# Kernel tuning notes

Hardware: AMD Instinct MI355X
Metric: run time of the kernel (lower is better)

Reference implementation:

```python
import jax, jax.numpy as jnp
import numpy as np

VOL = 64          # self.vol_size
SPACE = 0.2       # space_size (cubic), space_center = 0
IMG = 255.0       # normalization constant in the source (2*u/255 - 1)


def setup_inputs() -> dict:
    key = jax.random.key(0)
    ks = jax.random.split(key, 5)
    B, V, C, Hf, Wf = 2, 4, 32, 64, 64
    features = jax.random.normal(ks[0], (B, V, C, Hf, Wf), jnp.float32)
    # near-identity rotations, cameras ~0.5m away, focal ~200, principal point 128
    camera_R = jnp.eye(3, dtype=jnp.float32)[None, None] + 0.01 * jax.random.normal(ks[1], (B, V, 3, 3), jnp.float32)
    camera_T = jnp.array([0.0, 0.0, 0.5], jnp.float32) + 0.01 * jax.random.normal(ks[2], (B, V, 3), jnp.float32)
    K0 = jnp.array([[200.0, 0.0, 128.0], [0.0, 200.0, 128.0], [0.0, 0.0, 1.0]], jnp.float32)
    Kmask = jnp.array([[1.0, 0.0, 1.0], [0.0, 1.0, 1.0], [0.0, 0.0, 0.0]], jnp.float32)
    camera_K = K0[None, None] + 0.5 * jax.random.normal(ks[3], (B, V, 3, 3), jnp.float32) * Kmask
    root_world = 0.01 * jax.random.normal(ks[4], (B, 3), jnp.float32)
    return dict(features=features, camera_R=camera_R, camera_T=camera_T,
                camera_K=camera_K, root_world=root_world)


def _bilinear_sample(feat, x, y):
    """PyTorch F.grid_sample, mode=bilinear, padding=zeros, align_corners=False.
    feat: [N,C,H,W]; x,y: [N,P] pixel-space coords (already unnormalized).
    Returns [N,C,P]."""
    N, C, H, W = feat.shape
    x0 = jnp.floor(x); y0 = jnp.floor(y)
    x1 = x0 + 1.0;     y1 = y0 + 1.0
    wx1 = x - x0; wx0 = 1.0 - wx1
    wy1 = y - y0; wy0 = 1.0 - wy1
    feat_flat = feat.reshape(N, C, H * W)

    def gather(xi, yi, w):
        valid = (xi >= 0) & (xi <= W - 1) & (yi >= 0) & (yi <= H - 1)
        xi_c = jnp.clip(xi, 0, W - 1).astype(jnp.int32)
        yi_c = jnp.clip(yi, 0, H - 1).astype(jnp.int32)
        idx = yi_c * W + xi_c                                   # [N,P]
        vals = jnp.take_along_axis(feat_flat, idx[:, None, :], axis=2)  # [N,C,P]
        return vals * (w * valid.astype(feat.dtype))[:, None, :]

    return (gather(x0, y0, wx0 * wy0) + gather(x1, y0, wx1 * wy0)
            + gather(x0, y1, wx0 * wy1) + gather(x1, y1, wx1 * wy1))


def reference(features, camera_R, camera_T, camera_K, root_world):
    B, V, C, Hf, Wf = features.shape
    D = VOL
    # _build_grid: 64^3 points, xyz order, spanning SPACE around center 0
    r = jnp.arange(D, dtype=jnp.float32)
    z, y, x = jnp.meshgrid(r, r, r, indexing='ij')
    grid = jnp.stack([x, y, z], axis=0) / (D - 1)               # [3,D,D,D]
    pts = ((grid - 0.5) * SPACE).reshape(3, -1).T               # [P,3], P = D^3
    # relative camera translation: new_T = R @ root + T
    new_T = jnp.einsum('bvij,bj->bvi', camera_R, root_world) + camera_T
    # project: pts_cam = pts @ R^T + T  -> [B,V,P,3]
    pts_cam = jnp.einsum('pj,bvij->bvpi', pts, camera_R) + new_T[:, :, None, :]
    zc = jnp.maximum(pts_cam[..., 2], 1e-5)
    fx = camera_K[:, :, 0, 0][..., None]; fy = camera_K[:, :, 1, 1][..., None]
    cx = camera_K[:, :, 0, 2][..., None]; cy = camera_K[:, :, 1, 2][..., None]
    u = pts_cam[..., 0] * fx / zc + cx
    v = pts_cam[..., 1] * fy / zc + cy
    u_n = 2.0 * u / IMG - 1.0
    v_n = 2.0 * v / IMG - 1.0
    # unnormalize (align_corners=False): ix = ((g+1)*W - 1)/2
    px = ((u_n + 1.0) * Wf - 1.0) * 0.5
    py = ((v_n + 1.0) * Hf - 1.0) * 0.5
    feat_bv = features.reshape(B * V, C, Hf, Wf)
    vol = _bilinear_sample(feat_bv, px.reshape(B * V, -1), py.reshape(B * V, -1))  # [BV,C,P]
    vol = vol.reshape(B, V, C, D, D, D).mean(axis=1)            # average over views
    return vol
```

## Files before the change

### kernel.cpp

```cpp
#include <hip/hip_runtime.h>

#define B_   2
#define V_   4
#define C_   32
#define HW_  4096
#define D_   64
#define P_   (D_*D_*D_)
#define SCL_ (64.0f/255.0f)

#define TXv_ 16
#define TYv_ 4
#define TZv_ 4
#define WCAP_ 10
#define HCAP_ 6
#define SLOTS_   64
#define SSTRIDE_ 80
#define STEP_ (0.2f/63.0f)

typedef _Float16 half2v __attribute__((ext_vector_type(2)));
typedef __fp16  fp16x2 __attribute__((ext_vector_type(2)));

union Corner32 { uint4 u[2]; half2v h[8]; };
union H2U { half2v h; fp16x2 f; unsigned int u; };

__global__ __launch_bounds__(256) void tx_kernel(const float* __restrict__ in,
                                                 unsigned int* __restrict__ out) {
    __shared__ float tile[32][65];
    const int bv  = blockIdx.x >> 6;
    const int hw0 = (blockIdx.x & 63) << 6;
    const int t   = threadIdx.x;
    const float* src = in + (size_t)bv * C_ * HW_ + hw0;
#pragma unroll
    for (int i = 0; i < 8; ++i) {
        int e = t + (i << 8);
        tile[e >> 6][e & 63] = src[(e >> 6) * HW_ + (e & 63)];
    }
    __syncthreads();
    unsigned int* dst = out + ((size_t)bv * HW_ + hw0) * (C_ / 2);
#pragma unroll
    for (int i = 0; i < 4; ++i) {
        int idx = t + (i << 8);
        int c  = (idx << 1) & 31;
        int hw = idx >> 4;
        half2v v = { (_Float16)tile[c][hw], (_Float16)tile[c + 1][hw] };
        dst[idx] = *(unsigned int*)&v;
    }
}

__device__ __forceinline__ void gather_blend(
    const unsigned char* __restrict__ vb,
    float px, float py, int rx0, int ry0, int W,
    half2v* __restrict__ acc)
{
    const float x0f = floorf(px), y0f = floorf(py);
    const float wx1 = px - x0f, wx0 = 1.0f - wx1;
    const float wy1 = py - y0f, wy0 = 1.0f - wy1;
    const float x1f = x0f + 1.0f, y1f = y0f + 1.0f;
    const float vx0 = (x0f >= 0.0f && x0f <= 63.0f) ? 0.25f : 0.0f;
    const float vx1 = (x1f >= 0.0f && x1f <= 63.0f) ? 0.25f : 0.0f;
    const float vy0 = (y0f >= 0.0f && y0f <= 63.0f) ? 1.0f : 0.0f;
    const float vy1 = (y1f >= 0.0f && y1f <= 63.0f) ? 1.0f : 0.0f;
    const float w00 = wx0*wy0*vx0*vy0, w01 = wx1*wy0*vx1*vy0;
    const float w10 = wx0*wy1*vx0*vy1, w11 = wx1*wy1*vx1*vy1;
    H2U u0, u1, u2, u3;
    u0.f = __builtin_amdgcn_cvt_pkrtz(w00, w00);
    u1.f = __builtin_amdgcn_cvt_pkrtz(w01, w01);
    u2.f = __builtin_amdgcn_cvt_pkrtz(w10, w10);
    u3.f = __builtin_amdgcn_cvt_pkrtz(w11, w11);

    const int x0c = (int)fminf(fmaxf(x0f, 0.0f), 63.0f);
    const int x1c = (int)fminf(fmaxf(x1f, 0.0f), 63.0f);
    const int y0c = (int)fminf(fmaxf(y0f, 0.0f), 63.0f);
    const int y1c = (int)fminf(fmaxf(y1f, 0.0f), 63.0f);
    const int dx0 = x0c - rx0, dx1 = x1c - rx0;
    const int r0 = (y0c - ry0) * W, r1 = (y1c - ry0) * W;
    const int o00 = (r0 + dx0) * SSTRIDE_, o01 = (r0 + dx1) * SSTRIDE_;
    const int o10 = (r1 + dx0) * SSTRIDE_, o11 = (r1 + dx1) * SSTRIDE_;

    Corner32 c00, c01, c10, c11;
    c00.u[0] = *(const uint4*)(vb + o00); c00.u[1] = *(const uint4*)(vb + o00 + 16);
    c01.u[0] = *(const uint4*)(vb + o01); c01.u[1] = *(const uint4*)(vb + o01 + 16);
    c10.u[0] = *(const uint4*)(vb + o10); c10.u[1] = *(const uint4*)(vb + o10 + 16);
    c11.u[0] = *(const uint4*)(vb + o11); c11.u[1] = *(const uint4*)(vb + o11 + 16);
#pragma unroll
    for (int j = 0; j < 8; ++j) {
        acc[j] += c00.h[j] * u0.h;
        acc[j] += c01.h[j] * u1.h;
        acc[j] += c10.h[j] * u2.h;
        acc[j] += c11.h[j] * u3.h;
    }
}

__global__ __launch_bounds__(256, 4) void vol_kernel(
    const unsigned char* __restrict__ feat,
    const float* __restrict__ Rm,
    const float* __restrict__ Tm,
    const float* __restrict__ Km,
    const float* __restrict__ root,
    float* __restrict__ out)
{
    __shared__ __align__(16) float cam[4][20];
    __shared__ __align__(16) int   srect[4][8];
    __shared__ __align__(16) unsigned char sfeat[4][SLOTS_ * SSTRIDE_];

    const int t = threadIdx.x;
    const int b = blockIdx.x >> 10;
    const int tile = blockIdx.x & 1023;
    const int gx0 = (tile & 3) << 4;
    const int gy0 = ((tile >> 2) & 15) << 2;
    const int gz0 = (tile >> 6) << 2;

    if (t < 32) {
        const int v = t & 3, c = t >> 2;
        const int bv = b * V_ + v;
        const float* Rb = Rm + bv * 9;
        const float* Tb = Tm + bv * 3;
        const float* Kb = Km + bv * 9;
        const float rx = root[b*3+0], ry = root[b*3+1], rz = root[b*3+2];
        const float r00=Rb[0], r01=Rb[1], r02=Rb[2];
        const float r10=Rb[3], r11=Rb[4], r12=Rb[5];
        const float r20=Rb[6], r21=Rb[7], r22=Rb[8];
        const float t0 = r00*rx + r01*ry + r02*rz + Tb[0];
        const float t1 = r10*rx + r11*ry + r12*rz + Tb[1];
        const float t2 = r20*rx + r21*ry + r22*rz + Tb[2];
        const float fx = Kb[0] * SCL_, fy = Kb[4] * SCL_;
        const float cx = Kb[2] * SCL_ - 0.5f, cy = Kb[5] * SCL_ - 0.5f;

        const float X = (float)(gx0 + (c & 1) * (TXv_-1)) * STEP_ - 0.1f;
        const float Y = (float)(gy0 + ((c >> 1) & 1) * (TYv_-1)) * STEP_ - 0.1f;
        const float Z = (float)(gz0 + (c >> 2) * (TZv_-1)) * STEP_ - 0.1f;
        const float xc = r00*X + r01*Y + r02*Z + t0;
        const float yc = r10*X + r11*Y + r12*Z + t1;
        float zc       = r20*X + r21*Y + r22*Z + t2;
        zc = fmaxf(zc, 1e-5f);
        const float inv = __builtin_amdgcn_rcpf(zc);
        float px = (xc * inv) * fx + cx;
        float py = (yc * inv) * fy + cy;

        float pxmn = px, pxmx = px, pymn = py, pymx = py;
#pragma unroll
        for (int m = 4; m <= 16; m <<= 1) {
            pxmn = fminf(pxmn, __shfl_xor(pxmn, m));
            pxmx = fmaxf(pxmx, __shfl_xor(pxmx, m));
            pymn = fminf(pymn, __shfl_xor(pymn, m));
            pymx = fmaxf(pymx, __shfl_xor(pymx, m));
        }
        if (c == 0) {
            cam[v][0] = r00; cam[v][1] = r01; cam[v][2] = r02; cam[v][3] = t0;
            cam[v][4] = r10; cam[v][5] = r11; cam[v][6] = r12; cam[v][7] = t1;
            cam[v][8] = r20; cam[v][9] = r21; cam[v][10] = r22; cam[v][11] = t2;
            cam[v][12] = fx; cam[v][13] = fy; cam[v][14] = cx; cam[v][15] = cy;
            const float dZ = 2.0f * STEP_;
            cam[v][16] = r02 * dZ; cam[v][17] = r12 * dZ; cam[v][18] = r22 * dZ;
            int rx0 = (int)floorf(pxmn); rx0 = max(0, min(63, rx0));
            int rx1 = (int)floorf(pxmx) + 1; rx1 = max(rx0, min(63, rx1));
            const int W = min(rx1 - rx0 + 1, WCAP_);
            int ry0 = (int)floorf(pymn); ry0 = max(0, min(63, ry0));
            int ry1 = (int)floorf(pymx) + 1; ry1 = max(ry0, min(63, ry1));
            const int H = min(ry1 - ry0 + 1, HCAP_);
            srect[v][0] = rx0; srect[v][1] = ry0; srect[v][2] = W; srect[v][3] = H;
            srect[v][4] = 65536 / W + 1;
            srect[v][5] = W * H * 4;
        }
    }
    __syncthreads();

    const int bvb = b * V_;
#pragma unroll
    for (int v = 0; v < 4; ++v) {
        const int nch = srect[v][5];
        if (t < nch) {
            const int rx0 = srect[v][0], ry0 = srect[v][1];
            const int W = srect[v][2], M = srect[v][4];
            const int part = t & 3, pi = t >> 2;
            const int dy = (pi * M) >> 16;
            const int dx = pi - dy * W;
            const unsigned char* src = feat + (size_t)(bvb + v) * HW_ * 64;
            const uint4 val = *(const uint4*)(src
                + (size_t)(((ry0 + dy) << 6) + rx0 + dx) * 64 + part * 16);
            *(uint4*)&sfeat[v][pi * SSTRIDE_ + part * 16] = val;
        }
    }
    __syncthreads();

    const int h = t & 1;
    const int vx = t >> 1;
    const float X = (float)(gx0 + (vx & 15)) * STEP_ - 0.1f;
    const float Y = (float)(gy0 + ((vx >> 4) & 3)) * STEP_ - 0.1f;
    const float Z = (float)(gz0 + (vx >> 6)) * STEP_ - 0.1f;

    const half2v z2h = { (_Float16)0.0f, (_Float16)0.0f };
    half2v accA[8], accB[8];
#pragma unroll
    for (int j = 0; j < 8; ++j) { accA[j] = z2h; accB[j] = z2h; }

#pragma unroll
    for (int v = 0; v < 4; ++v) {
        const float4 cA = *(const float4*)&cam[v][0];
        const float4 cB = *(const float4*)&cam[v][4];
        const float4 cC = *(const float4*)&cam[v][8];
        const float4 cK = *(const float4*)&cam[v][12];
        const float dxz = cam[v][16], dyz = cam[v][17], dzz = cam[v][18];
        const int rx0 = srect[v][0], ry0 = srect[v][1], W = srect[v][2];
        const unsigned char* vb = &sfeat[v][0] + (h << 5);

        const float xcA = cA.x*X + cA.y*Y + cA.z*Z + cA.w;
        const float ycA = cB.x*X + cB.y*Y + cB.z*Z + cB.w;
        const float zcA = cC.x*X + cC.y*Y + cC.z*Z + cC.w;
        const float xcB = xcA + dxz, ycB = ycA + dyz, zcB = zcA + dzz;

        const float invA = __builtin_amdgcn_rcpf(fmaxf(zcA, 1e-5f));
        const float invB = __builtin_amdgcn_rcpf(fmaxf(zcB, 1e-5f));
        const float pxA = (xcA * invA) * cK.x + cK.z;
        const float pyA = (ycA * invA) * cK.y + cK.w;
        const float pxB = (xcB * invB) * cK.x + cK.z;
        const float pyB = (ycB * invB) * cK.y + cK.w;

        gather_blend(vb, pxA, pyA, rx0, ry0, W, accA);
        gather_blend(vb, pxB, pyB, rx0, ry0, W, accB);
    }

    const int gx = gx0 + (vx & 15);
    const int gy = gy0 + ((vx >> 4) & 3);
    const int gz = gz0 + (vx >> 6);
    const int p = (((gz << 6) + gy) << 6) + gx;
    float* ob = out + ((size_t)(b * C_) + (h << 4)) * P_ + p;
#pragma unroll
    for (int j = 0; j < 8; ++j) {
        __builtin_nontemporal_store((float)accA[j].x, ob + (size_t)(2*j  ) * P_);
        __builtin_nontemporal_store((float)accA[j].y, ob + (size_t)(2*j+1) * P_);
        __builtin_nontemporal_store((float)accB[j].x, ob + (size_t)(2*j  ) * P_ + 8192);
        __builtin_nontemporal_store((float)accB[j].y, ob + (size_t)(2*j+1) * P_ + 8192);
    }
}

__global__ __launch_bounds__(256) void vol_fallback(
    const float* __restrict__ feat,
    const float* __restrict__ Rm, const float* __restrict__ Tm,
    const float* __restrict__ Km, const float* __restrict__ root,
    float* __restrict__ out)
{
    const int b = blockIdx.x >> 10;
    const int p = ((blockIdx.x & 1023) << 8) | threadIdx.x;
    const int xi = p & 63, yi = (p >> 6) & 63, zi = p >> 12;
    const float X = ((float)xi * (1.0f/63.0f) - 0.5f) * 0.2f;
    const float Y = ((float)yi * (1.0f/63.0f) - 0.5f) * 0.2f;
    const float Z = ((float)zi * (1.0f/63.0f) - 0.5f) * 0.2f;
    float acc[C_];
#pragma unroll
    for (int c = 0; c < C_; ++c) acc[c] = 0.0f;
    const float rx = root[b*3+0], ry = root[b*3+1], rz = root[b*3+2];
#pragma unroll
    for (int v = 0; v < V_; ++v) {
        const int bv = b * V_ + v;
        const float* Rb = Rm + bv * 9; const float* Tb = Tm + bv * 3;
        const float* Kb = Km + bv * 9;
        const float r00=Rb[0], r01=Rb[1], r02=Rb[2];
        const float r10=Rb[3], r11=Rb[4], r12=Rb[5];
        const float r20=Rb[6], r21=Rb[7], r22=Rb[8];
        const float t0 = r00*rx + r01*ry + r02*rz + Tb[0];
        const float t1 = r10*rx + r11*ry + r12*rz + Tb[1];
        const float t2 = r20*rx + r21*ry + r22*rz + Tb[2];
        const float xc = r00*X + r01*Y + r02*Z + t0;
        const float yc = r10*X + r11*Y + r12*Z + t1;
        float zc       = r20*X + r21*Y + r22*Z + t2;
        zc = fmaxf(zc, 1e-5f);
        const float inv = 1.0f / zc;
        const float px = xc * (Kb[0]*SCL_) * inv + (Kb[2]*SCL_ - 0.5f);
        const float py = yc * (Kb[4]*SCL_) * inv + (Kb[5]*SCL_ - 0.5f);
        const float x0f = floorf(px), y0f = floorf(py);
        const float wx1 = px - x0f, wx0 = 1.0f - wx1;
        const float wy1 = py - y0f, wy0 = 1.0f - wy1;
        const float x1f = x0f + 1.0f, y1f = y0f + 1.0f;
        const float vx0 = (x0f >= 0.0f && x0f <= 63.0f) ? 1.0f : 0.0f;
        const float vx1 = (x1f >= 0.0f && x1f <= 63.0f) ? 1.0f : 0.0f;
        const float vy0 = (y0f >= 0.0f && y0f <= 63.0f) ? 1.0f : 0.0f;
        const float vy1 = (y1f >= 0.0f && y1f <= 63.0f) ? 1.0f : 0.0f;
        const float w00 = wx0*wy0*vx0*vy0, w01 = wx1*wy0*vx1*vy0;
        const float w10 = wx0*wy1*vx0*vy1, w11 = wx1*wy1*vx1*vy1;
        const int x0c = (int)fminf(fmaxf(x0f, 0.0f), 63.0f);
        const int x1c = (int)fminf(fmaxf(x1f, 0.0f), 63.0f);
        const int y0c = (int)fminf(fmaxf(y0f, 0.0f), 63.0f);
        const int y1c = (int)fminf(fmaxf(y1f, 0.0f), 63.0f);
        const float* fb = feat + (size_t)bv * C_ * HW_;
        const int i00 = y0c*64 + x0c, i01 = y0c*64 + x1c;
        const int i10 = y1c*64 + x0c, i11 = y1c*64 + x1c;
#pragma unroll
        for (int c = 0; c < C_; ++c) {
            const float* f = fb + c * HW_;
            acc[c] += w00*f[i00] + w01*f[i01] + w10*f[i10] + w11*f[i11];
        }
    }
    float* ob = out + (size_t)b * C_ * P_ + p;
#pragma unroll
    for (int c = 0; c < C_; ++c) ob[(size_t)c * P_] = acc[c] * 0.25f;
}

extern "C" void kernel_launch(void* const* d_in, const int* in_sizes, int n_in,
                              void* d_out, int out_size, void* d_ws, size_t ws_size,
                              hipStream_t stream) {
    const float* feat = (const float*)d_in[0];
    const float* Rm   = (const float*)d_in[1];
    const float* Tm   = (const float*)d_in[2];
    const float* Km   = (const float*)d_in[3];
    const float* root = (const float*)d_in[4];
    float* out = (float*)d_out;

    const size_t need = (size_t)B_ * V_ * HW_ * C_ * sizeof(_Float16);
    if (ws_size >= need) {
        unsigned int* ftx = (unsigned int*)d_ws;
        tx_kernel<<<B_ * V_ * 64, 256, 0, stream>>>(feat, ftx);
        vol_kernel<<<B_ * 1024, 256, 0, stream>>>(
            (const unsigned char*)ftx, Rm, Tm, Km, root, out);
    } else {
        vol_fallback<<<B_ * P_ / 256, 256, 0, stream>>>(feat, Rm, Tm, Km, root, out);
    }
}
```

Before: 95.64 us.

## Fuse fp32-to-fp16 transpose into volume kernel's shared-memory staging

Drops the separate transpose kernel that converted features into a channel-interleaved fp16 workspace. Each volume block now reads the fp32 channel-planar features for its footprint rectangle directly, converts them to fp16 and packs them into shared memory itself. This saves one kernel launch and the workspace write and read-back. In exchange the staging loads are strided per channel (8 scalar loads per thread, spaced one plane apart), and the workspace-size fallback path is removed.

```diff
diff --git a/kernel.cpp b/kernel.cpp
--- a/kernel.cpp
+++ b/kernel.cpp
@@ -22,30 +22,6 @@
 
 union Corner32 { uint4 u[2]; half2v h[8]; };
 union H2U { half2v h; fp16x2 f; unsigned int u; };
-
-__global__ __launch_bounds__(256) void tx_kernel(const float* __restrict__ in,
-                                                 unsigned int* __restrict__ out) {
-    __shared__ float tile[32][65];
-    const int bv  = blockIdx.x >> 6;
-    const int hw0 = (blockIdx.x & 63) << 6;
-    const int t   = threadIdx.x;
-    const float* src = in + (size_t)bv * C_ * HW_ + hw0;
-#pragma unroll
-    for (int i = 0; i < 8; ++i) {
-        int e = t + (i << 8);
-        tile[e >> 6][e & 63] = src[(e >> 6) * HW_ + (e & 63)];
-    }
-    __syncthreads();
-    unsigned int* dst = out + ((size_t)bv * HW_ + hw0) * (C_ / 2);
-#pragma unroll
-    for (int i = 0; i < 4; ++i) {
-        int idx = t + (i << 8);
-        int c  = (idx << 1) & 31;
-        int hw = idx >> 4;
-        half2v v = { (_Float16)tile[c][hw], (_Float16)tile[c + 1][hw] };
-        dst[idx] = *(unsigned int*)&v;
-    }
-}
 
 __device__ __forceinline__ void gather_blend(
     const unsigned char* __restrict__ vb,
@@ -91,8 +67,8 @@
     }
 }
 
-__global__ __launch_bounds__(256, 4) void vol_kernel(
-    const unsigned char* __restrict__ feat,
+__global__ __launch_bounds__(256, 4) void vol_fused(
+    const float* __restrict__ feat,
     const float* __restrict__ Rm,
     const float* __restrict__ Tm,
     const float* __restrict__ Km,
@@ -160,25 +136,42 @@
             const int H = min(ry1 - ry0 + 1, HCAP_);
             srect[v][0] = rx0; srect[v][1] = ry0; srect[v][2] = W; srect[v][3] = H;
             srect[v][4] = 65536 / W + 1;
-            srect[v][5] = W * H * 4;
+            srect[v][5] = W * H;
         }
     }
     __syncthreads();
 
     const int bvb = b * V_;
-#pragma unroll
-    for (int v = 0; v < 4; ++v) {
-        const int nch = srect[v][5];
-        if (t < nch) {
-            const int rx0 = srect[v][0], ry0 = srect[v][1];
-            const int W = srect[v][2], M = srect[v][4];
-            const int part = t & 3, pi = t >> 2;
-            const int dy = (pi * M) >> 16;
-            const int dx = pi - dy * W;
-            const unsigned char* src = feat + (size_t)(bvb + v) * HW_ * 64;
-            const uint4 val = *(const uint4*)(src
-                + (size_t)(((ry0 + dy) << 6) + rx0 + dx) * 64 + part * 16);
-            *(uint4*)&sfeat[v][pi * SSTRIDE_ + part * 16] = val;
+    {
+        const int slot = t & 63;
+        const int k    = t >> 6;
+#pragma unroll
+        for (int v = 0; v < 4; ++v) {
+            const int nsl = srect[v][5];
+            if (slot < nsl) {
+                const int rx0 = srect[v][0], ry0 = srect[v][1];
+                const int W = srect[v][2], M = srect[v][4];
+                const int dy = (slot * M) >> 16;
+                const int dx = slot - dy * W;
+                const int pix = ((ry0 + dy) << 6) + rx0 + dx;
+                const float* sp = feat + (size_t)(bvb + v) * (C_ * HW_)
+                                + (size_t)(k << 3) * HW_ + pix;
+                float f0 = sp[0];
+                float f1 = sp[HW_];
+                float f2 = sp[2 * HW_];
+                float f3 = sp[3 * HW_];
+                float f4 = sp[4 * HW_];
+                float f5 = sp[5 * HW_];
+                float f6 = sp[6 * HW_];
+                float f7 = sp[7 * HW_];
+                half2v h0 = { (_Float16)f0, (_Float16)f1 };
+                half2v h1 = { (_Float16)f2, (_Float16)f3 };
+                half2v h2 = { (_Float16)f4, (_Float16)f5 };
+                half2v h3 = { (_Float16)f6, (_Float16)f7 };
+                uint4 val = { *(unsigned int*)&h0, *(unsigned int*)&h1,
+                              *(unsigned int*)&h2, *(unsigned int*)&h3 };
+                *(uint4*)&sfeat[v][slot * SSTRIDE_ + (k << 4)] = val;
+            }
         }
     }
     __syncthreads();
@@ -232,68 +225,6 @@
         __builtin_nontemporal_store((float)accB[j].x, ob + (size_t)(2*j  ) * P_ + 8192);
         __builtin_nontemporal_store((float)accB[j].y, ob + (size_t)(2*j+1) * P_ + 8192);
     }
-}
-
-__global__ __launch_bounds__(256) void vol_fallback(
-    const float* __restrict__ feat,
-    const float* __restrict__ Rm, const float* __restrict__ Tm,
-    const float* __restrict__ Km, const float* __restrict__ root,
-    float* __restrict__ out)
-{
-    const int b = blockIdx.x >> 10;
-    const int p = ((blockIdx.x & 1023) << 8) | threadIdx.x;
-    const int xi = p & 63, yi = (p >> 6) & 63, zi = p >> 12;
-    const float X = ((float)xi * (1.0f/63.0f) - 0.5f) * 0.2f;
-    const float Y = ((float)yi * (1.0f/63.0f) - 0.5f) * 0.2f;
-    const float Z = ((float)zi * (1.0f/63.0f) - 0.5f) * 0.2f;
-    float acc[C_];
-#pragma unroll
-    for (int c = 0; c < C_; ++c) acc[c] = 0.0f;
-    const float rx = root[b*3+0], ry = root[b*3+1], rz = root[b*3+2];
-#pragma unroll
-    for (int v = 0; v < V_; ++v) {
-        const int bv = b * V_ + v;
-        const float* Rb = Rm + bv * 9; const float* Tb = Tm + bv * 3;
-        const float* Kb = Km + bv * 9;
-        const float r00=Rb[0], r01=Rb[1], r02=Rb[2];
-        const float r10=Rb[3], r11=Rb[4], r12=Rb[5];
-        const float r20=Rb[6], r21=Rb[7], r22=Rb[8];
-        const float t0 = r00*rx + r01*ry + r02*rz + Tb[0];
-        const float t1 = r10*rx + r11*ry + r12*rz + Tb[1];
-        const float t2 = r20*rx + r21*ry + r22*rz + Tb[2];
-        const float xc = r00*X + r01*Y + r02*Z + t0;
-        const float yc = r10*X + r11*Y + r12*Z + t1;
-        float zc       = r20*X + r21*Y + r22*Z + t2;
-        zc = fmaxf(zc, 1e-5f);
-        const float inv = 1.0f / zc;
-        const float px = xc * (Kb[0]*SCL_) * inv + (Kb[2]*SCL_ - 0.5f);
-        const float py = yc * (Kb[4]*SCL_) * inv + (Kb[5]*SCL_ - 0.5f);
-        const float x0f = floorf(px), y0f = floorf(py);
-        const float wx1 = px - x0f, wx0 = 1.0f - wx1;
-        const float wy1 = py - y0f, wy0 = 1.0f - wy1;
-        const float x1f = x0f + 1.0f, y1f = y0f + 1.0f;
-        const float vx0 = (x0f >= 0.0f && x0f <= 63.0f) ? 1.0f : 0.0f;
-        const float vx1 = (x1f >= 0.0f && x1f <= 63.0f) ? 1.0f : 0.0f;
-        const float vy0 = (y0f >= 0.0f && y0f <= 63.0f) ? 1.0f : 0.0f;
-        const float vy1 = (y1f >= 0.0f && y1f <= 63.0f) ? 1.0f : 0.0f;
-        const float w00 = wx0*wy0*vx0*vy0, w01 = wx1*wy0*vx1*vy0;
-        const float w10 = wx0*wy1*vx0*vy1, w11 = wx1*wy1*vx1*vy1;
-        const int x0c = (int)fminf(fmaxf(x0f, 0.0f), 63.0f);
-        const int x1c = (int)fminf(fmaxf(x1f, 0.0f), 63.0f);
-        const int y0c = (int)fminf(fmaxf(y0f, 0.0f), 63.0f);
-        const int y1c = (int)fminf(fmaxf(y1f, 0.0f), 63.0f);
-        const float* fb = feat + (size_t)bv * C_ * HW_;
-        const int i00 = y0c*64 + x0c, i01 = y0c*64 + x1c;
-        const int i10 = y1c*64 + x0c, i11 = y1c*64 + x1c;
-#pragma unroll
-        for (int c = 0; c < C_; ++c) {
-            const float* f = fb + c * HW_;
-            acc[c] += w00*f[i00] + w01*f[i01] + w10*f[i10] + w11*f[i11];
-        }
-    }
-    float* ob = out + (size_t)b * C_ * P_ + p;
-#pragma unroll
-    for (int c = 0; c < C_; ++c) ob[(size_t)c * P_] = acc[c] * 0.25f;
 }
 
 extern "C" void kernel_launch(void* const* d_in, const int* in_sizes, int n_in,
@@ -306,13 +237,6 @@
     const float* root = (const float*)d_in[4];
     float* out = (float*)d_out;
 
-    const size_t need = (size_t)B_ * V_ * HW_ * C_ * sizeof(_Float16);
-    if (ws_size >= need) {
-        unsigned int* ftx = (unsigned int*)d_ws;
-        tx_kernel<<<B_ * V_ * 64, 256, 0, stream>>>(feat, ftx);
-        vol_kernel<<<B_ * 1024, 256, 0, stream>>>(
-            (const unsigned char*)ftx, Rm, Tm, Km, root, out);
-    } else {
-        vol_fallback<<<B_ * P_ / 256, 256, 0, stream>>>(feat, Rm, Tm, Km, root, out);
-    }
+    (void)d_ws; (void)ws_size;
+    vol_fused<<<B_ * 1024, 256, 0, stream>>>(feat, Rm, Tm, Km, root, out);
 }
```

New measurement: 94.70 us. About the same (-1.0%).
